# Optimization experiments

Hardware: AMD Instinct MI355X
Metric: run time of the kernel (lower is better)

Reference implementation:

```python
import jax, jax.numpy as jnp
import numpy as np

N, E = 30000, 240000          # nodes, edges per view
IN, D, OUT = 512, 128, 64      # in_dim, hidden_dim, out_dim
V, BLK, H, DM = 2, 2, 2, 64    # num_view, blk_size, num_heads, gate max-pool dim
NEG_ATT, NEG_OUT = 0.2, 0.01   # leaky_relu slopes (attention / outer)


def setup_inputs() -> dict:
    key = jax.random.key(0)
    ks = jax.random.split(key, 12)
    s = 0.05
    f32 = jnp.float32
    return {
        "ft": jax.random.normal(ks[0], (N, IN), f32),
        "src": jax.random.randint(ks[1], (V, E), 0, N, jnp.int32),
        "dst": jax.random.randint(ks[2], (V, E), 0, N, jnp.int32),
        "W_proj": jax.random.normal(ks[3], (IN, D), f32) * s,
        "W_embed": jax.random.normal(ks[4], (D, D), f32) * s,
        "a_l": jax.random.normal(ks[5], (V, BLK, H, D), f32) * s,
        "a_r": jax.random.normal(ks[6], (V, BLK, H, D), f32) * s,
        "Wv": jax.random.normal(ks[7], (V, BLK, H, D, D), f32) * s,
        "Wgm": jax.random.normal(ks[8], (V, BLK, D, DM), f32) * s,
        "Wgate": jax.random.normal(ks[9], (V, BLK, 2 * D + DM, H), f32) * s,
        "b_gate": jnp.zeros((V, BLK, H), f32),
        "W_tran": jax.random.normal(ks[10], (2 * D + DM and (D + V * H * D), OUT), f32) * s if False else jax.random.normal(ks[10], (D + V * H * D, OUT), f32) * s,
        "b_tran": jnp.zeros((OUT,), f32),
    }


def _seg_sum(x, idx):
    return jax.ops.segment_sum(x, idx, num_segments=N)


def _cgaan_layer(v, z, s_idx, d_idx, al, ar, wv, wgm, wgate, bg, merge):
    # v: [N,D] values, z: [N,D] attention features ('proj_z')
    # Multi-head attention logits: e_ij = leaky_relu(a_l.z_src + a_r.z_dst)  [E,H]
    logit_l = jnp.einsum("nd,hd->nh", z, al)
    logit_r = jnp.einsum("nd,hd->nh", z, ar)
    e = jax.nn.leaky_relu(logit_l[s_idx] + logit_r[d_idx], NEG_ATT)
    # edge softmax over incoming edges of each dst node
    m = jax.ops.segment_max(e, d_idx, num_segments=N)          # [N,H]
    ex = jnp.exp(e - m[d_idx])
    denom = _seg_sum(ex, d_idx)                                 # [N,H]
    alpha = ex / denom[d_idx]                                   # [E,H]
    # per-head value projection and weighted aggregation
    wvn = jnp.einsum("nd,hde->nhe", v, wv)                      # [N,H,D]
    agg = _seg_sum(alpha[:, :, None] * wvn[s_idx], d_idx)       # [N,H,D]
    # GaAN-style gate: sigmoid(FC([x_i, mean_j v_j, max_j (v_j Wgm)])) -> per-head scalar
    deg = _seg_sum(jnp.ones((s_idx.shape[0],), v.dtype), d_idx)  # [N]
    mean_n = _seg_sum(v[s_idx], d_idx) / jnp.maximum(deg, 1.0)[:, None]
    mx = jax.ops.segment_max((v @ wgm)[s_idx], d_idx, num_segments=N)
    mx = jnp.where(deg[:, None] > 0, mx, 0.0)                   # isolated nodes -> 0
    g = jax.nn.sigmoid(jnp.concatenate([v, mean_n, mx], -1) @ wgate + bg)  # [N,H]
    agg = g[:, :, None] * agg
    if merge == "mean":
        return agg.mean(axis=1)                                 # [N,D]
    return agg.reshape(agg.shape[0], -1)                        # cat -> [N,H*D]


def reference(ft, src, dst, W_proj, W_embed, a_l, a_r, Wv, Wgm, Wgate, b_gate, W_tran, b_tran):
    proj = ft @ W_proj                                          # [N,D]
    cur = [proj for _ in range(V)]
    for i in range(BLK):
        merge = "mean" if i < BLK - 1 else "cat"
        nxt = []
        for j in range(V):
            z = cur[j] @ W_embed
            h = _cgaan_layer(cur[j], z, src[j], dst[j], a_l[j, i], a_r[j, i],
                             Wv[j, i], Wgm[j, i], Wgate[j, i], b_gate[j, i], merge)
            nxt.append(jax.nn.leaky_relu(h, NEG_OUT))
        cur = nxt
    h = jnp.concatenate([proj] + cur, axis=-1)                  # [N, D+V*H*D]
    return h @ W_tran + b_tran
```

## Files before the change

### kernel.cpp

```cpp
#include <hip/hip_runtime.h>
#include <hip/hip_bf16.h>
#include <math.h>

#define NN 30000
#define EE 240000
#define IN_DIM 512
#define DD 128
#define OUTD 64
#define NV 2
#define NBLK 2
#define NH 2
#define DMM 64
#define NEG_ATT 0.2f
#define NEG_OUT 0.01f
#define CH 1024
#define NCH ((NN + CH - 1) / CH)

typedef __attribute__((ext_vector_type(8))) short bf16x8;
typedef __attribute__((ext_vector_type(4))) float f32x4;
typedef __attribute__((ext_vector_type(4))) unsigned short us4;
typedef __attribute__((ext_vector_type(8))) unsigned short us8;

#define OFF_PROJVM 0
#define OFF_WV     131072
#define OFF_WGM    262144
#define OFF_TRAN   278528
#define WT_TOTAL   319488

__device__ __forceinline__ unsigned split_bf(float x) {
  unsigned u = __float_as_uint(x);
  unsigned hb = (u + 0x7FFFu + ((u >> 16) & 1u)) >> 16;
  float hf = __uint_as_float(hb << 16);
  float lo = x - hf;
  unsigned ul = __float_as_uint(lo);
  unsigned lb = (ul + 0x7FFFu + ((ul >> 16) & 1u)) >> 16;
  return hb | (lb << 16);
}
__device__ __forceinline__ unsigned short f2bf(float x) {
  unsigned u = __float_as_uint(x);
  return (unsigned short)((u + 0x7FFFu + ((u >> 16) & 1u)) >> 16);
}
__device__ __forceinline__ float bf2f(unsigned short u) {
  return __uint_as_float((unsigned)u << 16);
}
__device__ __forceinline__ void gload16(void* lds, const void* g) {
  __builtin_amdgcn_global_load_lds((const __attribute__((address_space(1))) unsigned int*)g,
                                   (__attribute__((address_space(3))) unsigned int*)lds, 16, 0, 0);
}

__global__ __launch_bounds__(256) void kA_deg_prepw(const int* __restrict__ dst, int* __restrict__ deg,
                                                    const float* __restrict__ W_embed,
                                                    const float* __restrict__ a_l, const float* __restrict__ a_r,
                                                    const float* __restrict__ Wp, const float* __restrict__ Wgm,
                                                    float* __restrict__ Bl, float* __restrict__ Br,
                                                    float* __restrict__ wf) {
  int b = blockIdx.x;
  if (b < 1875) {
    int e = b * 256 + threadIdx.x;
    if (e < NV * EE) atomicAdd(&deg[(e / EE) * NN + dst[e]], 1);
    return;
  }
  int pb = b - 1875;
  if (pb < 256) {
    int idx = pb * 256 + threadIdx.x;
    int j = idx >> 15, k = (idx >> 6) & 511, n = idx & 63;
    const float* wp = Wp + (size_t)k * DD;
    const float* wg = Wgm + (size_t)(j * NBLK + 0) * DD * DMM + n;
    float s = 0.f;
    for (int e = 0; e < DD; e++) s += wp[e] * wg[(size_t)e * DMM];
    wf[idx] = s;
  } else {
    int idx = (pb - 256) * 256 + threadIdx.x;
    if (idx >= NV * NBLK * DD * NH) return;
    int h = idx & 1, dd = (idx >> 1) & 127, lv = idx >> 8;
    const float* w = W_embed + dd * DD;
    const float* al = a_l + (lv * NH + h) * DD;
    const float* ar = a_r + (lv * NH + h) * DD;
    float sl = 0.f, sr = 0.f;
    for (int e = 0; e < DD; e++) { float we = w[e]; sl += we * al[e]; sr += we * ar[e]; }
    Bl[idx] = sl; Br[idx] = sr;
  }
}

__global__ __launch_bounds__(256) void kB_scan1_wsplit(const int* __restrict__ deg, int* __restrict__ partial,
                                                       const float* __restrict__ Wp, const float* __restrict__ wf,
                                                       const float* __restrict__ Wv, const float* __restrict__ Wgm,
                                                       const float* __restrict__ Wt,
                                                       unsigned short* __restrict__ hi,
                                                       unsigned short* __restrict__ lo) {
  int b = blockIdx.x;
  if (b < 60) {
    int view = b / NCH, ch = b % NCH;
    const int* d = deg + view * NN + ch * CH;
    int rem = min(CH, NN - ch * CH);
    int t = threadIdx.x;
    int s = 0;
    for (int i = t; i < rem; i += 256) s += d[i];
    for (int k = 32; k; k >>= 1) s += __shfl_xor(s, k);
    __shared__ int wsum[4];
    if ((t & 63) == 0) wsum[t >> 6] = s;
    __syncthreads();
    if (t == 0) partial[b] = wsum[0] + wsum[1] + wsum[2] + wsum[3];
    return;
  }
  int wb = b - 60;
  const int pre[11] = {0, 256, 384, 512, 640, 768, 896, 1024, 1056, 1088, 1248};
  int y = 0;
  while (y < 10 && wb >= pre[y + 1]) y++;
  int bx = wb - pre[y];
  const float* src; int K, N; size_t doff;
  if (y == 0)      { src = Wp;                      K = 512; N = 128; doff = OFF_PROJVM; }
  else if (y <= 2) { int j = y - 1; src = wf + (size_t)j * 512 * 64; K = 512; N = 64; doff = OFF_PROJVM + (size_t)(128 + j * 64) * 512; }
  else if (y <= 6) { int lv = y - 3; src = Wv + (size_t)lv * 32768;  K = 256; N = 128; doff = OFF_WV + (size_t)lv * 32768; }
  else if (y <= 8) { int j = y - 7; src = Wgm + (size_t)(j * NBLK + 1) * 8192; K = 128; N = 64; doff = OFF_WGM + (size_t)j * 8192; }
  else             { src = Wt;                      K = 640; N = 64;  doff = OFF_TRAN; }
  int idx = bx * 256 + threadIdx.x;
  if (idx >= K * N) return;
  int n = idx / K, k = idx % K;
  int tk = k >> 6, g = (k >> 3) & 7, j2 = k & 7;
  int ks = (tk << 6) | ((g ^ (n & 7)) << 3) | j2;
  unsigned p = split_bf(src[(size_t)k * N + n]);
  hi[doff + (size_t)n * K + ks] = (unsigned short)(p & 0xFFFFu);
  lo[doff + (size_t)n * K + ks] = (unsigned short)(p >> 16);
}

__global__ void k_scan2(const int* __restrict__ partial, int* __restrict__ chunkoff, int* __restrict__ off) {
  if (threadIdx.x == 0 && blockIdx.x == 0) {
    for (int v = 0; v < NV; v++) {
      int acc = 0;
      for (int c = 0; c < NCH; c++) { chunkoff[v * NCH + c] = acc; acc += partial[v * NCH + c]; }
      off[v * (NN + 1) + NN] = acc;
    }
  }
}

__global__ __launch_bounds__(256) void k_scan3(const int* __restrict__ deg, const int* __restrict__ chunkoff,
                                               int* __restrict__ off) {
  int b = blockIdx.x, view = b / NCH, ch = b % NCH;
  int base = ch * CH;
  const int* d = deg + view * NN;
  int* o = off + view * (NN + 1);
  int t = threadIdx.x, lane = t & 63, w = t >> 6;
  int i0 = base + t * 4;
  int x0 = 0, x1 = 0, x2 = 0, x3 = 0;
  if (i0 + 3 < NN) { int4 q = *(const int4*)(d + i0); x0 = q.x; x1 = q.y; x2 = q.z; x3 = q.w; }
  else {
    if (i0     < NN) x0 = d[i0];
    if (i0 + 1 < NN) x1 = d[i0 + 1];
    if (i0 + 2 < NN) x2 = d[i0 + 2];
  }
  int tot = x0 + x1 + x2 + x3;
  int incl = tot;
  for (int k = 1; k < 64; k <<= 1) { int y = __shfl_up(incl, k); if (lane >= k) incl += y; }
  __shared__ int wt[4];
  if (lane == 63) wt[w] = incl;
  __syncthreads();
  int wexcl = 0;
  for (int k = 0; k < w; k++) wexcl += wt[k];
  int excl = chunkoff[b] + wexcl + incl - tot;
  if (i0     < NN) o[i0]     = excl;
  if (i0 + 1 < NN) o[i0 + 1] = excl + x0;
  if (i0 + 2 < NN) o[i0 + 2] = excl + x0 + x1;
  if (i0 + 3 < NN) o[i0 + 3] = excl + x0 + x1 + x2;
}

__global__ __launch_bounds__(256) void k_fill(const int* __restrict__ src, const int* __restrict__ dst,
                                              const int* __restrict__ off, int* __restrict__ cursor,
                                              int* __restrict__ csr_src) {
  int e = blockIdx.x * 256 + threadIdx.x;
  if (e >= NV * EE) return;
  int view = e / EE;
  int d = dst[e];
  int p = atomicAdd(&cursor[view * NN + d], 1);
  csr_src[view * EE + off[view * (NN + 1) + d] + p] = src[e];
}

__global__ __launch_bounds__(256) void k_llr(const unsigned short* __restrict__ p0,
                                             const unsigned short* __restrict__ p1, int ps,
                                             const float* __restrict__ Bl0, const float* __restrict__ Br0,
                                             const float* __restrict__ Bl1, const float* __restrict__ Br1,
                                             const float* __restrict__ Wg0, const float* __restrict__ Wg1,
                                             float4* __restrict__ lq, float2* __restrict__ lr) {
  int lane = threadIdx.x & 63, wid = threadIdx.x >> 6;
  int n = blockIdx.x * 4 + wid;
  int k = lane * 2;
  unsigned a = *(const unsigned*)(p0 + (size_t)n * ps + k);
  unsigned b = *(const unsigned*)(p1 + (size_t)n * ps + k);
  float ax = bf2f((unsigned short)a), ay = bf2f((unsigned short)(a >> 16));
  float bx = bf2f((unsigned short)b), by = bf2f((unsigned short)(b >> 16));
  float r[12];
  r[0]  = ax * Bl0[k * 2]     + ay * Bl0[k * 2 + 2];
  r[1]  = ax * Bl0[k * 2 + 1] + ay * Bl0[k * 2 + 3];
  r[2]  = ax * Br0[k * 2]     + ay * Br0[k * 2 + 2];
  r[3]  = ax * Br0[k * 2 + 1] + ay * Br0[k * 2 + 3];
  r[4]  = ax * Wg0[(128 + k) * 2]     + ay * Wg0[(129 + k) * 2];
  r[5]  = ax * Wg0[(128 + k) * 2 + 1] + ay * Wg0[(129 + k) * 2 + 1];
  r[6]  = bx * Bl1[k * 2]     + by * Bl1[k * 2 + 2];
  r[7]  = bx * Bl1[k * 2 + 1] + by * Bl1[k * 2 + 3];
  r[8]  = bx * Br1[k * 2]     + by * Br1[k * 2 + 2];
  r[9]  = bx * Br1[k * 2 + 1] + by * Br1[k * 2 + 3];
  r[10] = bx * Wg1[(128 + k) * 2]     + by * Wg1[(129 + k) * 2];
  r[11] = bx * Wg1[(128 + k) * 2 + 1] + by * Wg1[(129 + k) * 2 + 1];
  for (int s = 32; s; s >>= 1)
#pragma unroll
    for (int q = 0; q < 12; q++) r[q] += __shfl_xor(r[q], s);
  if (lane == 0) {
    lq[n] = make_float4(r[0], r[1], r[4], r[5]);
    lr[n] = make_float2(r[2], r[3]);
    lq[NN + n] = make_float4(r[6], r[7], r[10], r[11]);
    lr[NN + n] = make_float2(r[8], r[9]);
  }
}

__global__ __launch_bounds__(256) void k_edge(const int* __restrict__ off_, const int* __restrict__ csr_,
                                              const float4* __restrict__ lq_, const float2* __restrict__ lr_,
                                              const unsigned short* __restrict__ pk_, long viewStride,
                                              int ps, int vmoff0, int vmstep,
                                              const float* __restrict__ Wg_, const float* __restrict__ bg_,
                                              unsigned short* __restrict__ S_) {
  int view = blockIdx.y;
  const int* off = off_ + view * (NN + 1);
  const int* csr = csr_ + (size_t)view * EE;
  const float4* lq = lq_ + (size_t)view * NN;
  const float2* lrp = lr_ + (size_t)view * NN;
  const unsigned short* pk = pk_ + (size_t)view * viewStride;
  int vmoff = vmoff0 + view * vmstep;
  const float* Wg = Wg_ + (size_t)view * NBLK * (2 * DD + DMM) * NH;
  const float* bg = bg_ + view * NBLK * NH;
  unsigned short* S = S_ + (size_t)view * NN * 256;

  int lane = threadIdx.x & 63, wid = threadIdx.x >> 6;
  int n = blockIdx.x * 4 + wid;
  int e0 = off[n], nb = off[n + 1] - e0;
  int q4 = lane >> 4, l16 = lane & 15;
  if (nb == 0) {
    if (lane < 32) {
      us8 z8 = {0, 0, 0, 0, 0, 0, 0, 0};
      *(us8*)(S + (size_t)n * 256 + q4 * 128 + l16 * 8) = z8;
    }
    return;
  }
  float2 lrn = lrp[n];
  float sa0[8] = {0.f}, sa1[8] = {0.f};
  float vmm[4] = {-INFINITY, -INFINITY, -INFINITY, -INFINITY};
  float d0 = 0.f, d1 = 0.f, tm0 = 0.f, tm1 = 0.f;
  for (int base = 0; base < nb; base += 64) {
    int i = base + lane;
    float w0 = 0.f, w1 = 0.f; int sidx = 0;
    if (i < nb) {
      sidx = csr[e0 + i];
      float4 qq = lq[sidx];
      float x0 = qq.x + lrn.x, x1 = qq.y + lrn.y;
      x0 = (x0 > 0.f) ? x0 : NEG_ATT * x0;
      x1 = (x1 > 0.f) ? x1 : NEG_ATT * x1;
      w0 = __expf(x0); w1 = __expf(x1);
      d0 += w0; d1 += w1; tm0 += qq.z; tm1 += qq.w;
    }
    int cnt = min(64, nb - base);
    for (int s = 0; 4 * s < cnt; s++) {
      int j = 4 * s + q4;
      if (j < cnt) {
        int se = __shfl(sidx, j);
        float we0 = __shfl(w0, j), we1 = __shfl(w1, j);
        const unsigned short* rowp = pk + (size_t)se * ps;
        us8 vq = *(const us8*)(rowp + l16 * 8);
#pragma unroll
        for (int k = 0; k < 8; k++) {
          float v = bf2f(vq[k]);
          sa0[k] += we0 * v; sa1[k] += we1 * v;
        }
        us4 vmq = *(const us4*)(rowp + vmoff + l16 * 4);
#pragma unroll
        for (int k = 0; k < 4; k++) vmm[k] = fmaxf(vmm[k], bf2f(vmq[k]));
      }
    }
  }
#pragma unroll
  for (int k = 0; k < 8; k++) {
    sa0[k] += __shfl_xor(sa0[k], 16); sa0[k] += __shfl_xor(sa0[k], 32);
    sa1[k] += __shfl_xor(sa1[k], 16); sa1[k] += __shfl_xor(sa1[k], 32);
  }
#pragma unroll
  for (int k = 0; k < 4; k++) {
    vmm[k] = fmaxf(vmm[k], __shfl_xor(vmm[k], 16));
    vmm[k] = fmaxf(vmm[k], __shfl_xor(vmm[k], 32));
  }
  for (int s = 32; s; s >>= 1) { d0 += __shfl_xor(d0, s); d1 += __shfl_xor(d1, s); }
  unsigned vnu = *(const unsigned*)(pk + (size_t)n * ps + 2 * lane);
  float vnx = bf2f((unsigned short)vnu), vny = bf2f((unsigned short)(vnu >> 16));
  float im = 1.f / (float)nb;
  float p0 = vnx * Wg[(2 * lane) * 2]     + vny * Wg[(2 * lane + 1) * 2]     + tm0 * im;
  float p1 = vnx * Wg[(2 * lane) * 2 + 1] + vny * Wg[(2 * lane + 1) * 2 + 1] + tm1 * im;
  if (q4 == 1) {
#pragma unroll
    for (int k = 0; k < 4; k++) {
      int d = l16 * 4 + k;
      p0 += vmm[k] * Wg[(256 + d) * 2];
      p1 += vmm[k] * Wg[(256 + d) * 2 + 1];
    }
  }
  for (int s = 32; s; s >>= 1) { p0 += __shfl_xor(p0, s); p1 += __shfl_xor(p1, s); }
  float g0 = 1.f / (1.f + __expf(-(p0 + bg[0])));
  float g1 = 1.f / (1.f + __expf(-(p1 + bg[1])));
  float q0 = g0 / d0, q1 = g1 / d1;
  if (lane < 32) {
    const float* sp = q4 ? sa1 : sa0;
    float qq = q4 ? q1 : q0;
    us8 o8;
#pragma unroll
    for (int k = 0; k < 8; k++) o8[k] = f2bf(sp[k] * qq);
    *(us8*)(S + (size_t)n * 256 + q4 * 128 + l16 * 8) = o8;
  }
}

struct GB {
  const void* A[4];
  unsigned long long bofs[4];
  float* C[4];
  unsigned short* P[4];
  int ldc[4];
  int pldc[4];
};

template <int BN, bool ABF>
__global__ __launch_bounds__(256) void gemm_mfma(
    GB gb, const unsigned short* __restrict__ Bth, const unsigned short* __restrict__ Btl,
    int lda, int ldb, int M, int K,
    const float* __restrict__ bias, float fs, int flags) {
  constexpr int NSUB = BN / 32;
  constexpr int CPW = BN / 32;
  __shared__ __align__(16) unsigned short Ah[64][64];
  __shared__ __align__(16) unsigned short Bh[BN][64], Bl[BN][64];
  const int z = blockIdx.z, xb = blockIdx.x;
  const float* __restrict__ Af = (const float*)gb.A[z];
  const unsigned short* __restrict__ Ab = (const unsigned short*)gb.A[z];
  float* __restrict__ C = gb.C[z];
  unsigned short* __restrict__ P = gb.P[z];
  const int ldc = gb.ldc[z], pldc = gb.pldc[z];
  const size_t bofs = gb.bofs[z];
  const int t = threadIdx.x;
  const int lane = t & 63, wv = t >> 6;
  const int lm = lane & 15, lg = lane >> 4;
  const int m0w = (wv & 1) * 32, n0w = (wv >> 1) * (BN / 2);
  const int row0 = xb * 64;
  f32x4 acc[2][NSUB];
#pragma unroll
  for (int ms = 0; ms < 2; ms++)
#pragma unroll
    for (int ns = 0; ns < NSUB; ns++) acc[ms][ns] = (f32x4)0.f;

  float4 apre[2][2];
  const int ar_ = t >> 3, ag_ = t & 7;

  auto loadA = [&](int k0) {
    if constexpr (!ABF) {
#pragma unroll
      for (int q = 0; q < 2; q++) {
        int rr = row0 + q * 32 + ar_;
        if (rr < M) {
          const float* p = Af + (size_t)rr * lda + k0 + ag_ * 8;
          apre[q][0] = *(const float4*)p;
          apre[q][1] = *(const float4*)(p + 4);
        } else {
          apre[q][0] = make_float4(0.f, 0.f, 0.f, 0.f);
          apre[q][1] = make_float4(0.f, 0.f, 0.f, 0.f);
        }
      }
    }
  };
  auto storeA = [&]() {
    if constexpr (!ABF) {
#pragma unroll
      for (int q = 0; q < 2; q++) {
        int r = q * 32 + ar_;
        us8 h8;
        float vals[8] = {apre[q][0].x, apre[q][0].y, apre[q][0].z, apre[q][0].w,
                         apre[q][1].x, apre[q][1].y, apre[q][1].z, apre[q][1].w};
#pragma unroll
        for (int e = 0; e < 8; e++) h8[e] = f2bf(vals[e]);
        int c = (ag_ ^ (r & 7)) << 3;
        *(us8*)&Ah[r][c] = h8;
      }
    }
  };
  auto stageA_bf = [&](int k0) {
    if constexpr (ABF) {
#pragma unroll
      for (int q = 0; q < 2; q++) {
        int r = q * 32 + ar_;
        int rr = min(row0 + r, M - 1);
        int scg = ag_ ^ (r & 7);
        gload16((char*)&Ah[0][0] + q * 4096 + t * 16,
                Ab + (size_t)rr * lda + k0 + scg * 8);
      }
    }
  };
  auto stageB = [&](int k0) {
#pragma unroll
    for (int q = 0; q < CPW; q++) {
      int chunk = wv * CPW + q;
      int o = chunk * 1024 + lane * 16;
      int n = o >> 7;
      int pq = (o >> 4) & 7;
      size_t gofs = bofs + (size_t)n * ldb + k0 + pq * 8;
      gload16((char*)&Bh[0][0] + o, Bth + gofs);
      gload16((char*)&Bl[0][0] + o, Btl + gofs);
    }
  };

  loadA(0);
  for (int k0 = 0; k0 < K; k0 += 64) {
    if constexpr (ABF) stageA_bf(k0); else storeA();
    stageB(k0);
    __syncthreads();
    if constexpr (!ABF) { if (k0 + 64 < K) loadA(k0 + 64); }
#pragma unroll
    for (int kc = 0; kc < 2; kc++) {
      bf16x8 afh[2], bfh[NSUB], bfl[NSUB];
#pragma unroll
      for (int ms = 0; ms < 2; ms++) {
        int R = m0w + ms * 16 + lm;
        int c = (((kc * 4 + lg) ^ (R & 7)) << 3);
        afh[ms] = *(const bf16x8*)&Ah[R][c];
      }
#pragma unroll
      for (int ns = 0; ns < NSUB; ns++) {
        int R = n0w + ns * 16 + lm;
        int c = (((kc * 4 + lg) ^ (R & 7)) << 3);
        bfh[ns] = *(const bf16x8*)&Bh[R][c];
        bfl[ns] = *(const bf16x8*)&Bl[R][c];
      }
#pragma unroll
      for (int ms = 0; ms < 2; ms++)
#pragma unroll
        for (int ns = 0; ns < NSUB; ns++) {
          acc[ms][ns] = __builtin_amdgcn_mfma_f32_16x16x32_bf16(afh[ms], bfl[ns], acc[ms][ns], 0, 0, 0);
          acc[ms][ns] = __builtin_amdgcn_mfma_f32_16x16x32_bf16(afh[ms], bfh[ns], acc[ms][ns], 0, 0, 0);
        }
    }
    __syncthreads();
  }
#pragma unroll
  for (int ms = 0; ms < 2; ms++)
#pragma unroll
    for (int ns = 0; ns < NSUB; ns++)
#pragma unroll
      for (int j = 0; j < 4; j++) {
        int row = row0 + m0w + ms * 16 + lg * 4 + j;
        if (row >= M) continue;
        int col = n0w + ns * 16 + lm;
        float val = acc[ms][ns][j] * fs;
        if (bias) val += bias[col];
        if (flags & 2) val = (val > 0.f) ? val : NEG_OUT * val;
        if (C) C[(size_t)row * ldc + col] = val;
        if (P) P[(size_t)row * pldc + col] = f2bf(val);
      }
}

extern "C" void kernel_launch(void* const* d_in, const int* in_sizes, int n_in,
                              void* d_out, int out_size, void* d_ws, size_t ws_size,
                              hipStream_t stream) {
  const float* ft      = (const float*)d_in[0];
  const int*   src     = (const int*)  d_in[1];
  const int*   dst     = (const int*)  d_in[2];
  const float* W_proj  = (const float*)d_in[3];
  const float* W_embed = (const float*)d_in[4];
  const float* a_l     = (const float*)d_in[5];
  const float* a_r     = (const float*)d_in[6];
  const float* Wv      = (const float*)d_in[7];
  const float* Wgm     = (const float*)d_in[8];
  const float* Wgate   = (const float*)d_in[9];
  const float* b_gate  = (const float*)d_in[10];
  const float* W_tran  = (const float*)d_in[11];
  const float* b_tran  = (const float*)d_in[12];
  float* out = (float*)d_out;
  char* ws = (char*)d_ws;
  (void)in_sizes; (void)n_in; (void)out_size; (void)ws_size;

  size_t o = 0;
  auto take = [&](size_t bytes) { size_t r = o; o += (bytes + 255) & ~(size_t)255; return r; };
  int*   deg     = (int*)(ws + take((size_t)NV * NN * 4));
  int*   cursor  = (int*)(ws + take((size_t)NV * NN * 4));
  int*   csr_off = (int*)(ws + take((size_t)NV * (NN + 1) * 4));
  int*   csr_src = (int*)(ws + take((size_t)NV * EE * 4));
  int*   partial = (int*)(ws + take((size_t)NV * NCH * 4));
  int*   chunkoff= (int*)(ws + take((size_t)NV * NCH * 4));
  float* Bl      = (float*)(ws + take((size_t)NV * NBLK * DD * NH * 4));
  float* Br      = (float*)(ws + take((size_t)NV * NBLK * DD * NH * 4));
  float* wf      = (float*)(ws + take((size_t)NV * 512 * 64 * 4));
  unsigned short* whi = (unsigned short*)(ws + take((size_t)WT_TOTAL * 2));
  unsigned short* wlo = (unsigned short*)(ws + take((size_t)WT_TOTAL * 2));
  float* h       = (float*)(ws + take((size_t)NN * 640 * 4));
  unsigned short* pk0 = (unsigned short*)(ws + take((size_t)NN * 256 * 2));
  unsigned short* pk1 = (unsigned short*)(ws + take((size_t)NV * NN * 192 * 2));
  unsigned short* Sbf = (unsigned short*)(ws + take((size_t)NV * NN * 256 * 2));
  float4* lqb    = (float4*)(ws + take((size_t)NV * NN * 16));
  float2* lrb    = (float2*)(ws + take((size_t)NV * NN * 8));

  const int HSTR = 640;

  hipMemsetAsync(deg, 0, (size_t)(((size_t)NV * NN * 4 + 255) & ~(size_t)255) + (size_t)NV * NN * 4, stream);
  kA_deg_prepw<<<2135, 256, 0, stream>>>(dst, deg, W_embed, a_l, a_r, W_proj, Wgm, Bl, Br, wf);
  kB_scan1_wsplit<<<1308, 256, 0, stream>>>(deg, partial, W_proj, wf, Wv, Wgm, W_tran, whi, wlo);
  k_scan2<<<1, 64, 0, stream>>>(partial, chunkoff, csr_off);
  k_scan3<<<NV * NCH, 256, 0, stream>>>(deg, chunkoff, csr_off);
  k_fill<<<(NV * EE + 255) / 256, 256, 0, stream>>>(src, dst, csr_off, cursor, csr_src);

  const int GM = (NN + 63) / 64;

  {
    GB gb = {};
    gb.A[0] = ft; gb.A[1] = ft;
    gb.bofs[0] = OFF_PROJVM; gb.bofs[1] = OFF_PROJVM + (size_t)128 * 512;
    gb.C[0] = h;  gb.ldc[0] = HSTR;
    gb.P[0] = pk0;       gb.pldc[0] = 256;
    gb.P[1] = pk0 + 128; gb.pldc[1] = 256;
    gemm_mfma<128, false><<<dim3(GM, 1, 2), 256, 0, stream>>>(gb, whi, wlo, IN_DIM, 512, NN, 512,
                                                              nullptr, 1.f, 0);
  }

  k_llr<<<NN / 4, 256, 0, stream>>>(pk0, pk0, 256,
                                    Bl + 0 * 256, Br + 0 * 256, Bl + 2 * 256, Br + 2 * 256,
                                    Wgate, Wgate + (size_t)NBLK * 320 * NH,
                                    lqb, lrb);
  k_edge<<<dim3(NN / 4, 2), 256, 0, stream>>>(csr_off, csr_src, lqb, lrb,
                                              pk0, 0L, 256, 128, 64,
                                              Wgate, b_gate, Sbf);
  {
    GB gb = {};
    for (int j = 0; j < 2; j++) {
      gb.A[j] = Sbf + (size_t)j * NN * 256;
      gb.bofs[j] = OFF_WV + (size_t)(j * 2) * 32768;
      gb.P[j] = pk1 + (size_t)j * NN * 192;
      gb.pldc[j] = 192;
    }
    gemm_mfma<128, true><<<dim3(GM, 1, 2), 256, 0, stream>>>(gb, whi, wlo, 256, 256, NN, 256,
                                                             nullptr, 0.5f, 2);
  }
  {
    GB gb = {};
    for (int j = 0; j < 2; j++) {
      gb.A[j] = pk1 + (size_t)j * NN * 192;
      gb.bofs[j] = OFF_WGM + (size_t)j * 8192;
      gb.P[j] = pk1 + (size_t)j * NN * 192 + 128;
      gb.pldc[j] = 192;
    }
    gemm_mfma<64, true><<<dim3(GM, 1, 2), 256, 0, stream>>>(gb, whi, wlo, 192, 128, NN, 128,
                                                            nullptr, 1.f, 0);
  }
  k_llr<<<NN / 4, 256, 0, stream>>>(pk1, pk1 + (size_t)NN * 192, 192,
                                    Bl + 1 * 256, Br + 1 * 256, Bl + 3 * 256, Br + 3 * 256,
                                    Wgate + 640, Wgate + (size_t)NBLK * 640 + 640,
                                    lqb, lrb);
  k_edge<<<dim3(NN / 4, 2), 256, 0, stream>>>(csr_off, csr_src, lqb, lrb,
                                              pk1, (long)NN * 192, 192, 128, 0,
                                              Wgate + 640, b_gate + NH, Sbf);
  {
    GB gb = {};
    for (int z = 0; z < 4; z++) {
      int j = z >> 1, hd = z & 1;
      gb.A[z] = Sbf + (size_t)j * NN * 256 + hd * 128;
      gb.bofs[z] = OFF_WV + (size_t)(j * 2 + 1) * 32768 + hd * 128;
      gb.C[z] = h + 128 + z * 128;
      gb.ldc[z] = HSTR;
    }
    gemm_mfma<128, true><<<dim3(GM, 1, 4), 256, 0, stream>>>(gb, whi, wlo, 256, 256, NN, 128,
                                                             nullptr, 1.f, 2);
  }
  {
    GB gb = {};
    gb.A[0] = h; gb.bofs[0] = OFF_TRAN; gb.C[0] = out; gb.ldc[0] = OUTD;
    gemm_mfma<64, false><<<dim3(GM, 1, 1), 256, 0, stream>>>(gb, whi, wlo, HSTR, 640, NN, 640,
                                                             b_tran, 1.f, 0);
  }
}
```

Before: 341.6 us.

## Remap edge aggregation to two edges per step with software-prefetched row loads

The per-node aggregation kernel now splits the wavefront into two halves of 32 lanes, each handling one edge per step with 4 features per lane, where before it used four quarters of 16 lanes with 8 features per lane. The row loads for the next edge are issued before the current accumulation, a software-pipelined prefetch meant to hide gather latency. Fewer parallel edges per step means more serial iterations per node, and the final cross-lane reduction shrinks to one shuffle level. The prefetch clamps its index at 63 and masks the max-pool with a validity flag, so it may issue redundant loads past the end of the edge list.

New measurement: 325.1 us. 4.8% less time.

```diff
diff --git a/kernel.cpp b/kernel.cpp
--- a/kernel.cpp
+++ b/kernel.cpp
@@ -232,18 +232,15 @@
   int lane = threadIdx.x & 63, wid = threadIdx.x >> 6;
   int n = blockIdx.x * 4 + wid;
   int e0 = off[n], nb = off[n + 1] - e0;
-  int q4 = lane >> 4, l16 = lane & 15;
+  int half = lane >> 5, hl = lane & 31;
   if (nb == 0) {
-    if (lane < 32) {
-      us8 z8 = {0, 0, 0, 0, 0, 0, 0, 0};
-      *(us8*)(S + (size_t)n * 256 + q4 * 128 + l16 * 8) = z8;
-    }
+    us4 z4 = {0, 0, 0, 0};
+    *(us4*)(S + (size_t)n * 256 + half * 128 + 4 * hl) = z4;
     return;
   }
   float2 lrn = lrp[n];
-  float sa0[8] = {0.f}, sa1[8] = {0.f};
-  float vmm[4] = {-INFINITY, -INFINITY, -INFINITY, -INFINITY};
-  float d0 = 0.f, d1 = 0.f, tm0 = 0.f, tm1 = 0.f;
+  float sa0[4] = {0.f, 0.f, 0.f, 0.f}, sa1[4] = {0.f, 0.f, 0.f, 0.f};
+  float d0 = 0.f, d1 = 0.f, tm0 = 0.f, tm1 = 0.f, vm0 = -INFINITY, vm1 = -INFINITY;
   for (int base = 0; base < nb; base += 64) {
     int i = base + lane;
     float w0 = 0.f, w1 = 0.f; int sidx = 0;
@@ -257,60 +254,61 @@
       d0 += w0; d1 += w1; tm0 += qq.z; tm1 += qq.w;
     }
     int cnt = min(64, nb - base);
-    for (int s = 0; 4 * s < cnt; s++) {
-      int j = 4 * s + q4;
-      if (j < cnt) {
-        int se = __shfl(sidx, j);
-        float we0 = __shfl(w0, j), we1 = __shfl(w1, j);
-        const unsigned short* rowp = pk + (size_t)se * ps;
-        us8 vq = *(const us8*)(rowp + l16 * 8);
-#pragma unroll
-        for (int k = 0; k < 8; k++) {
-          float v = bf2f(vq[k]);
-          sa0[k] += we0 * v; sa1[k] += we1 * v;
-        }
-        us4 vmq = *(const us4*)(rowp + vmoff + l16 * 4);
-#pragma unroll
-        for (int k = 0; k < 4; k++) vmm[k] = fmaxf(vmm[k], bf2f(vmq[k]));
-      }
-    }
-  }
-#pragma unroll
-  for (int k = 0; k < 8; k++) {
-    sa0[k] += __shfl_xor(sa0[k], 16); sa0[k] += __shfl_xor(sa0[k], 32);
-    sa1[k] += __shfl_xor(sa1[k], 16); sa1[k] += __shfl_xor(sa1[k], 32);
+    int steps = (cnt + 1) >> 1;
+    int j = half;
+    int se = __shfl(sidx, j);
+    float wa = __shfl(w0, j), wb = __shfl(w1, j);
+    const unsigned short* rp = pk + (size_t)se * ps;
+    us4 vq = *(const us4*)(rp + 4 * hl);
+    unsigned mu = *(const unsigned*)(rp + vmoff + 2 * hl);
+    bool ok = (j < cnt);
+    for (int s = 0; s < steps; s++) {
+      int j1 = 2 * (s + 1) + half;
+      int jc = min(j1, 63);
+      int se1 = __shfl(sidx, jc);
+      float wa1 = __shfl(w0, jc), wb1 = __shfl(w1, jc);
+      const unsigned short* rp1 = pk + (size_t)se1 * ps;
+      us4 vq1 = *(const us4*)(rp1 + 4 * hl);
+      unsigned mu1 = *(const unsigned*)(rp1 + vmoff + 2 * hl);
+      float v0 = bf2f(vq[0]), v1 = bf2f(vq[1]), v2 = bf2f(vq[2]), v3 = bf2f(vq[3]);
+      sa0[0] += wa * v0; sa0[1] += wa * v1; sa0[2] += wa * v2; sa0[3] += wa * v3;
+      sa1[0] += wb * v0; sa1[1] += wb * v1; sa1[2] += wb * v2; sa1[3] += wb * v3;
+      float mv0 = ok ? bf2f((unsigned short)mu) : -INFINITY;
+      float mv1 = ok ? bf2f((unsigned short)(mu >> 16)) : -INFINITY;
+      vm0 = fmaxf(vm0, mv0); vm1 = fmaxf(vm1, mv1);
+      vq = vq1; mu = mu1; wa = wa1; wb = wb1; ok = (j1 < cnt);
+    }
   }
 #pragma unroll
   for (int k = 0; k < 4; k++) {
-    vmm[k] = fmaxf(vmm[k], __shfl_xor(vmm[k], 16));
-    vmm[k] = fmaxf(vmm[k], __shfl_xor(vmm[k], 32));
-  }
+    sa0[k] += __shfl_xor(sa0[k], 32);
+    sa1[k] += __shfl_xor(sa1[k], 32);
+  }
+  vm0 = fmaxf(vm0, __shfl_xor(vm0, 32));
+  vm1 = fmaxf(vm1, __shfl_xor(vm1, 32));
   for (int s = 32; s; s >>= 1) { d0 += __shfl_xor(d0, s); d1 += __shfl_xor(d1, s); }
   unsigned vnu = *(const unsigned*)(pk + (size_t)n * ps + 2 * lane);
   float vnx = bf2f((unsigned short)vnu), vny = bf2f((unsigned short)(vnu >> 16));
   float im = 1.f / (float)nb;
   float p0 = vnx * Wg[(2 * lane) * 2]     + vny * Wg[(2 * lane + 1) * 2]     + tm0 * im;
   float p1 = vnx * Wg[(2 * lane) * 2 + 1] + vny * Wg[(2 * lane + 1) * 2 + 1] + tm1 * im;
-  if (q4 == 1) {
-#pragma unroll
-    for (int k = 0; k < 4; k++) {
-      int d = l16 * 4 + k;
-      p0 += vmm[k] * Wg[(256 + d) * 2];
-      p1 += vmm[k] * Wg[(256 + d) * 2 + 1];
-    }
+  if (half == 1) {
+    p0 += vm0 * Wg[(256 + 2 * hl) * 2]     + vm1 * Wg[(256 + 2 * hl + 1) * 2];
+    p1 += vm0 * Wg[(256 + 2 * hl) * 2 + 1] + vm1 * Wg[(256 + 2 * hl + 1) * 2 + 1];
   }
   for (int s = 32; s; s >>= 1) { p0 += __shfl_xor(p0, s); p1 += __shfl_xor(p1, s); }
   float g0 = 1.f / (1.f + __expf(-(p0 + bg[0])));
   float g1 = 1.f / (1.f + __expf(-(p1 + bg[1])));
   float q0 = g0 / d0, q1 = g1 / d1;
-  if (lane < 32) {
-    const float* sp = q4 ? sa1 : sa0;
-    float qq = q4 ? q1 : q0;
-    us8 o8;
-#pragma unroll
-    for (int k = 0; k < 8; k++) o8[k] = f2bf(sp[k] * qq);
-    *(us8*)(S + (size_t)n * 256 + q4 * 128 + l16 * 8) = o8;
-  }
+  us4 o4;
+  if (half == 0) {
+    o4[0] = f2bf(sa0[0] * q0); o4[1] = f2bf(sa0[1] * q0);
+    o4[2] = f2bf(sa0[2] * q0); o4[3] = f2bf(sa0[3] * q0);
+  } else {
+    o4[0] = f2bf(sa1[0] * q1); o4[1] = f2bf(sa1[1] * q1);
+    o4[2] = f2bf(sa1[2] * q1); o4[3] = f2bf(sa1[3] * q1);
+  }
+  *(us4*)(S + (size_t)n * 256 + half * 128 + 4 * hl) = o4;
 }
 
 struct GB {
```
